# Kernel tuning notes

Hardware: AMD Instinct MI355X
Metric: run time of the kernel (lower is better)

The kernel has to match this reference:

```python
import jax, jax.numpy as jnp
import numpy as np

B, T, N, C, K = 32, 16, 512, 128, 2


def setup_inputs() -> dict:
    key = jax.random.key(0)
    k1, k2, k3 = jax.random.split(key, 3)
    x = jax.random.normal(k1, (B, T, N, C), dtype=jnp.float32)
    adj = jax.random.uniform(k2, (B, N, N), dtype=jnp.float32)
    lambdas = jnp.ones((K,), dtype=jnp.float32)           # raw lambda params (init 1.0)
    thetas = jax.random.uniform(k3, (K, C, C), dtype=jnp.float32)  # torch.rand init
    return {"x": x, "adj": adj, "lambdas": lambdas, "thetas": thetas}


def _akgcn_layer(x, adj, lam_raw, theta):
    # x: [B,T,N,C], adj: [B,N,N]
    lam = 1.0 + jax.nn.relu(lam_raw)  # actual lambda
    h = jnp.einsum('btnc,cd->btnd', x, theta)
    eye = jnp.eye(adj.shape[-1], dtype=adj.dtype)
    v = ((2.0 * lam - 2.0) / lam) * eye + (2.0 / lam) * adj   # [B,N,N]
    v = v / jnp.sum(v, axis=-1, keepdims=True)                 # row-normalize
    out = jnp.einsum('bnm,btmd->btnd', v, h)                   # vectorized over T
    return jax.nn.relu(out)


def reference(x, adj, lambdas, thetas):
    hid = x
    for k in range(K):  # small fixed layer count
        hid = _akgcn_layer(hid, adj, lambdas[k], thetas[k])
    return jax.nn.relu(x) + jax.nn.sigmoid(hid)
```

## Files before the change

### kernel.cpp

```cpp
#include <hip/hip_runtime.h>
#include <hip/hip_bf16.h>

#define BB 32
#define TT 16
#define NNODE 512
#define CC 128

typedef __attribute__((ext_vector_type(8))) short bf16x8;
typedef __attribute__((ext_vector_type(4))) short short4_t;
typedef __attribute__((ext_vector_type(4))) float f32x4;

__device__ __forceinline__ short f2bf(float f) {
    __hip_bfloat16 h = __float2bfloat16(f);
    return *reinterpret_cast<short*>(&h);
}

#define GLD16(g, l)                                                          \
    __builtin_amdgcn_global_load_lds(                                        \
        (const __attribute__((address_space(1))) unsigned int*)(g),          \
        (__attribute__((address_space(3))) unsigned int*)(l), 16, 0, 0)

__global__ void invs_kernel(const float* __restrict__ adj,
                            const float* __restrict__ lambdas, int layer,
                            float* __restrict__ invs) {
    int gid = blockIdx.x * blockDim.x + threadIdx.x;
    int row = gid >> 6;
    int lane = gid & 63;
    const float* r = adj + (long)row * NNODE;
    float s = 0.f;
#pragma unroll
    for (int i = 0; i < NNODE / 64; ++i) s += r[lane + 64 * i];
#pragma unroll
    for (int o = 32; o; o >>= 1) s += __shfl_xor(s, o, 64);
    if (lane == 0) {
        float lamm1 = fmaxf(lambdas[layer], 0.f);
        invs[row] = 1.f / (s + lamm1);
    }
}

__global__ void prep_adj_kernel(const float* __restrict__ adj,
                                const float* __restrict__ invs,
                                const float* __restrict__ lambdas, int layer,
                                short* __restrict__ Abf) {
    long e = ((long)blockIdx.x * 256 + threadIdx.x) * 8;
    int m = (int)(e & (NNODE - 1));
    int n = (int)((e >> 9) & (NNODE - 1));
    int b = (int)(e >> 18);
    float lamm1 = fmaxf(lambdas[layer], 0.f);
    float s = invs[b * NNODE + n];
    float4 f0 = *(const float4*)(adj + e);
    float4 f1 = *(const float4*)(adj + e + 4);
    float vv[8] = {f0.x, f0.y, f0.z, f0.w, f1.x, f1.y, f1.z, f1.w};
#pragma unroll
    for (int j = 0; j < 8; ++j) vv[j] *= s;
    int d = n - m;
    if (d >= 0 && d < 8) vv[d] += lamm1 * s;
    bf16x8 o;
#pragma unroll
    for (int j = 0; j < 8; ++j) o[j] = f2bf(vv[j]);
    *(bf16x8*)(&Abf[e]) = o;
}

__global__ void prep_theta_kernel(const float* __restrict__ theta,
                                  short* __restrict__ thT) {
    int idx = blockIdx.x * 256 + threadIdx.x;
    int i = idx >> 7, k = idx & (CC - 1);
    thT[i * CC + k] = f2bf(theta[k * CC + i]);
}

__global__ __launch_bounds__(256) void gemm_theta_mfma(
    const float* __restrict__ X, const short* __restrict__ thT,
    short* __restrict__ Ht) {
    __shared__ short As[128 * 32];
    __shared__ short Bs[128 * 32];
    const int t = threadIdx.x;
    const long rowBase = (long)blockIdx.x * 128;
    const int w = t >> 6, ln = t & 63;
    const int lm = ln & 15, q = ln >> 4;
    const int wy = w >> 1, wx = w & 1;

    f32x4 acc[4][4] = {};

    const int rr = w * 32 + (ln >> 2);
    const int kc = (ln & 3) * 8;
    short* ldsB = Bs + w * 1024 + ln * 8;

    for (int k0 = 0; k0 < CC; k0 += 32) {
        __syncthreads();
        const short* gb = thT + rr * CC + k0 + kc;
        GLD16(gb, ldsB);
        GLD16(gb + 16 * CC, ldsB + 512);
#pragma unroll
        for (int i = 0; i < 4; ++i) {
            int v = i * 256 + t;
            int r = v >> 3, kq = v & 7;
            float4 f = *(const float4*)(X + (rowBase + r) * CC + k0 + kq * 4);
            short4_t s = {f2bf(f.x), f2bf(f.y), f2bf(f.z), f2bf(f.w)};
            *(short4_t*)(&As[r * 32 + kq * 4]) = s;
        }
        __syncthreads();

        bf16x8 a[4], b[4];
#pragma unroll
        for (int i = 0; i < 4; ++i)
            a[i] = *(const bf16x8*)(&As[(wy * 64 + i * 16 + lm) * 32 + q * 8]);
#pragma unroll
        for (int j = 0; j < 4; ++j)
            b[j] = *(const bf16x8*)(&Bs[(wx * 64 + j * 16 + lm) * 32 + q * 8]);
#pragma unroll
        for (int i = 0; i < 4; ++i)
#pragma unroll
            for (int j = 0; j < 4; ++j)
                acc[i][j] = __builtin_amdgcn_mfma_f32_16x16x32_bf16(
                    a[i], b[j], acc[i][j], 0, 0, 0);
    }

    const long bt = rowBase >> 9;
    const int mBase = (int)(rowBase & (NNODE - 1));
    short* Hb = Ht + bt * (long)(NNODE * CC);
#pragma unroll
    for (int i = 0; i < 4; ++i) {
        int m = mBase + wy * 64 + i * 16 + q * 4;
#pragma unroll
        for (int j = 0; j < 4; ++j) {
            int c = wx * 64 + j * 16 + lm;
            f32x4 v = acc[i][j];
            short4_t s = {f2bf(v[0]), f2bf(v[1]), f2bf(v[2]), f2bf(v[3])};
            *(short4_t*)(&Hb[(long)c * NNODE + m]) = s;
        }
    }
}

template <int FUSE>
__global__ __launch_bounds__(256) void gemm_agg_mfma(
    const short* __restrict__ Abf, const short* __restrict__ Ht,
    const float* __restrict__ x, float* __restrict__ Out) {
    __shared__ short As[128 * 32];
    __shared__ short Bs[128 * 32];
    const int t = threadIdx.x;
    const int bt = blockIdx.y;
    const int n0 = blockIdx.x * 128;
    const short* Ab = Abf + (long)(bt >> 4) * NNODE * NNODE + (long)n0 * NNODE;
    const short* Hb = Ht + (long)bt * NNODE * CC;
    const int w = t >> 6, ln = t & 63;
    const int lm = ln & 15, q = ln >> 4;
    const int wy = w >> 1, wx = w & 1;

    f32x4 acc[4][4] = {};

    const int rr = w * 32 + (ln >> 2);
    const int kc = (ln & 3) * 8;
    short* ldsA = As + w * 1024 + ln * 8;
    short* ldsB = Bs + w * 1024 + ln * 8;

    for (int k0 = 0; k0 < NNODE; k0 += 32) {
        __syncthreads();
        const short* ga = Ab + (long)rr * NNODE + k0 + kc;
        const short* gb = Hb + (long)rr * NNODE + k0 + kc;
        GLD16(ga, ldsA);
        GLD16(ga + 16 * NNODE, ldsA + 512);
        GLD16(gb, ldsB);
        GLD16(gb + 16 * NNODE, ldsB + 512);
        __syncthreads();

        bf16x8 a[4], b[4];
#pragma unroll
        for (int i = 0; i < 4; ++i)
            a[i] = *(const bf16x8*)(&As[(wy * 64 + i * 16 + lm) * 32 + q * 8]);
#pragma unroll
        for (int j = 0; j < 4; ++j)
            b[j] = *(const bf16x8*)(&Bs[(wx * 64 + j * 16 + lm) * 32 + q * 8]);
#pragma unroll
        for (int i = 0; i < 4; ++i)
#pragma unroll
            for (int j = 0; j < 4; ++j)
                acc[i][j] = __builtin_amdgcn_mfma_f32_16x16x32_bf16(
                    a[i], b[j], acc[i][j], 0, 0, 0);
    }

    const long obase = (long)bt * NNODE * CC;
#pragma unroll
    for (int i = 0; i < 4; ++i) {
        int n = n0 + wy * 64 + i * 16 + q * 4;
#pragma unroll
        for (int j = 0; j < 4; ++j) {
            int c = wx * 64 + j * 16 + lm;
#pragma unroll
            for (int r = 0; r < 4; ++r) {
                long idx = obase + (long)(n + r) * CC + c;
                float v = fmaxf(acc[i][j][r], 0.f);
                if (FUSE) {
                    Out[idx] = fmaxf(x[idx], 0.f) + 1.f / (1.f + __expf(-v));
                } else {
                    Out[idx] = v;
                }
            }
        }
    }
}

extern "C" void kernel_launch(void* const* d_in, const int* in_sizes, int n_in,
                              void* d_out, int out_size, void* d_ws,
                              size_t ws_size, hipStream_t stream) {
    const float* x = (const float*)d_in[0];
    const float* adj = (const float*)d_in[1];
    const float* lambdas = (const float*)d_in[2];
    const float* thetas = (const float*)d_in[3];
    float* out = (float*)d_out;

    float* invs = (float*)d_ws;
    short* thT = (short*)(invs + BB * NNODE);
    short* Abf = thT + CC * CC;
    short* Ht = Abf + (long)BB * NNODE * NNODE;

    dim3 blk(256);
    dim3 g_pre(4096);
    dim3 g_theta(2048);
    dim3 g_agg(NNODE / 128, BB * TT);

    invs_kernel<<<g_pre, blk, 0, stream>>>(adj, lambdas, 0, invs);
    prep_adj_kernel<<<g_pre, blk, 0, stream>>>(adj, invs, lambdas, 0, Abf);
    prep_theta_kernel<<<64, blk, 0, stream>>>(thetas, thT);
    gemm_theta_mfma<<<g_theta, blk, 0, stream>>>(x, thT, Ht);
    gemm_agg_mfma<0><<<g_agg, blk, 0, stream>>>(Abf, Ht, out, out);

    invs_kernel<<<g_pre, blk, 0, stream>>>(adj, lambdas, 1, invs);
    prep_adj_kernel<<<g_pre, blk, 0, stream>>>(adj, invs, lambdas, 1, Abf);
    prep_theta_kernel<<<64, blk, 0, stream>>>(thetas + CC * CC, thT);
    gemm_theta_mfma<<<g_theta, blk, 0, stream>>>(out, thT, Ht);
    gemm_agg_mfma<1><<<g_agg, blk, 0, stream>>>(Abf, Ht, x, out);
}
```

Before: 476.6 us.

## Fuse layer-1 aggregation with layer-2 theta GEMM and merge adjacency prep kernels

Merges the row-sum and normalize/convert kernels for the adjacency into one wave-per-row kernel, so adj is read once per layer instead of twice. Fuses the first aggregation GEMM with the second layer's theta GEMM: the ReLU'd tile is staged in LDS as bf16 and multiplied by theta2 in the same block. This removes the fp32 intermediate write and re-read and one full GEMM launch. It uses the output buffer as bf16 scratch for the first H, adds extra LDS (Ts tile), and adds one more rounding to bf16 of the intermediate.

```diff
diff --git a/kernel.cpp b/kernel.cpp
--- a/kernel.cpp
+++ b/kernel.cpp
@@ -20,45 +20,33 @@
         (const __attribute__((address_space(1))) unsigned int*)(g),          \
         (__attribute__((address_space(3))) unsigned int*)(l), 16, 0, 0)
 
-__global__ void invs_kernel(const float* __restrict__ adj,
-                            const float* __restrict__ lambdas, int layer,
-                            float* __restrict__ invs) {
+__global__ void prep_adj2_kernel(const float* __restrict__ adj,
+                                 const float* __restrict__ lambdas, int layer,
+                                 short* __restrict__ Abf) {
     int gid = blockIdx.x * blockDim.x + threadIdx.x;
     int row = gid >> 6;
     int lane = gid & 63;
+    int n = row & (NNODE - 1);
     const float* r = adj + (long)row * NNODE;
-    float s = 0.f;
-#pragma unroll
-    for (int i = 0; i < NNODE / 64; ++i) s += r[lane + 64 * i];
+    float4 f0 = *(const float4*)(r + lane * 4);
+    float4 f1 = *(const float4*)(r + 256 + lane * 4);
+    float s = f0.x + f0.y + f0.z + f0.w + f1.x + f1.y + f1.z + f1.w;
 #pragma unroll
     for (int o = 32; o; o >>= 1) s += __shfl_xor(s, o, 64);
-    if (lane == 0) {
-        float lamm1 = fmaxf(lambdas[layer], 0.f);
-        invs[row] = 1.f / (s + lamm1);
-    }
-}
-
-__global__ void prep_adj_kernel(const float* __restrict__ adj,
-                                const float* __restrict__ invs,
-                                const float* __restrict__ lambdas, int layer,
-                                short* __restrict__ Abf) {
-    long e = ((long)blockIdx.x * 256 + threadIdx.x) * 8;
-    int m = (int)(e & (NNODE - 1));
-    int n = (int)((e >> 9) & (NNODE - 1));
-    int b = (int)(e >> 18);
     float lamm1 = fmaxf(lambdas[layer], 0.f);
-    float s = invs[b * NNODE + n];
-    float4 f0 = *(const float4*)(adj + e);
-    float4 f1 = *(const float4*)(adj + e + 4);
-    float vv[8] = {f0.x, f0.y, f0.z, f0.w, f1.x, f1.y, f1.z, f1.w};
-#pragma unroll
-    for (int j = 0; j < 8; ++j) vv[j] *= s;
-    int d = n - m;
-    if (d >= 0 && d < 8) vv[d] += lamm1 * s;
-    bf16x8 o;
-#pragma unroll
-    for (int j = 0; j < 8; ++j) o[j] = f2bf(vv[j]);
-    *(bf16x8*)(&Abf[e]) = o;
+    float inv = 1.f / (s + lamm1);
+    float v[8] = {f0.x, f0.y, f0.z, f0.w, f1.x, f1.y, f1.z, f1.w};
+#pragma unroll
+    for (int j = 0; j < 8; ++j) v[j] *= inv;
+    int d0 = n - lane * 4;
+    if (d0 >= 0 && d0 < 4) v[d0] += lamm1 * inv;
+    int d1 = n - 256 - lane * 4;
+    if (d1 >= 0 && d1 < 4) v[4 + d1] += lamm1 * inv;
+    short* o = Abf + (long)row * NNODE;
+    short4_t s0 = {f2bf(v[0]), f2bf(v[1]), f2bf(v[2]), f2bf(v[3])};
+    short4_t s1 = {f2bf(v[4]), f2bf(v[5]), f2bf(v[6]), f2bf(v[7])};
+    *(short4_t*)(o + lane * 4) = s0;
+    *(short4_t*)(o + 256 + lane * 4) = s1;
 }
 
 __global__ void prep_theta_kernel(const float* __restrict__ theta,
@@ -127,6 +115,99 @@
             f32x4 v = acc[i][j];
             short4_t s = {f2bf(v[0]), f2bf(v[1]), f2bf(v[2]), f2bf(v[3])};
             *(short4_t*)(&Hb[(long)c * NNODE + m]) = s;
+        }
+    }
+}
+
+__global__ __launch_bounds__(256) void gemm_agg_theta(
+    const short* __restrict__ Abf, const short* __restrict__ Ht1,
+    const short* __restrict__ thT2, short* __restrict__ Ht2) {
+    __shared__ short As[128 * 32];
+    __shared__ short Bs[128 * 32];
+    __shared__ short Ts[128][136];
+    const int t = threadIdx.x;
+    const int bt = blockIdx.y;
+    const int n0 = blockIdx.x * 128;
+    const short* Ab = Abf + (long)(bt >> 4) * NNODE * NNODE + (long)n0 * NNODE;
+    const short* Hb = Ht1 + (long)bt * NNODE * CC;
+    const int w = t >> 6, ln = t & 63;
+    const int lm = ln & 15, q = ln >> 4;
+    const int wy = w >> 1, wx = w & 1;
+
+    f32x4 acc[4][4] = {};
+
+    const int rr = w * 32 + (ln >> 2);
+    const int kc = (ln & 3) * 8;
+    short* ldsA = As + w * 1024 + ln * 8;
+    short* ldsB = Bs + w * 1024 + ln * 8;
+
+    for (int k0 = 0; k0 < NNODE; k0 += 32) {
+        __syncthreads();
+        const short* ga = Ab + (long)rr * NNODE + k0 + kc;
+        const short* gb = Hb + (long)rr * NNODE + k0 + kc;
+        GLD16(ga, ldsA);
+        GLD16(ga + 16 * NNODE, ldsA + 512);
+        GLD16(gb, ldsB);
+        GLD16(gb + 16 * NNODE, ldsB + 512);
+        __syncthreads();
+
+        bf16x8 a[4], b[4];
+#pragma unroll
+        for (int i = 0; i < 4; ++i)
+            a[i] = *(const bf16x8*)(&As[(wy * 64 + i * 16 + lm) * 32 + q * 8]);
+#pragma unroll
+        for (int j = 0; j < 4; ++j)
+            b[j] = *(const bf16x8*)(&Bs[(wx * 64 + j * 16 + lm) * 32 + q * 8]);
+#pragma unroll
+        for (int i = 0; i < 4; ++i)
+#pragma unroll
+            for (int j = 0; j < 4; ++j)
+                acc[i][j] = __builtin_amdgcn_mfma_f32_16x16x32_bf16(
+                    a[i], b[j], acc[i][j], 0, 0, 0);
+    }
+
+#pragma unroll
+    for (int i = 0; i < 4; ++i)
+#pragma unroll
+        for (int j = 0; j < 4; ++j)
+#pragma unroll
+            for (int r = 0; r < 4; ++r)
+                Ts[wy * 64 + i * 16 + q * 4 + r][wx * 64 + j * 16 + lm] =
+                    f2bf(fmaxf(acc[i][j][r], 0.f));
+
+    f32x4 acc2[4][4] = {};
+    for (int c0 = 0; c0 < CC; c0 += 32) {
+        __syncthreads();
+        const short* gb = thT2 + rr * CC + c0 + kc;
+        GLD16(gb, ldsB);
+        GLD16(gb + 16 * CC, ldsB + 512);
+        __syncthreads();
+
+        bf16x8 a[4], b[4];
+#pragma unroll
+        for (int i = 0; i < 4; ++i)
+            a[i] = *(const bf16x8*)(&Ts[wy * 64 + i * 16 + lm][c0 + q * 8]);
+#pragma unroll
+        for (int j = 0; j < 4; ++j)
+            b[j] = *(const bf16x8*)(&Bs[(wx * 64 + j * 16 + lm) * 32 + q * 8]);
+#pragma unroll
+        for (int i = 0; i < 4; ++i)
+#pragma unroll
+            for (int j = 0; j < 4; ++j)
+                acc2[i][j] = __builtin_amdgcn_mfma_f32_16x16x32_bf16(
+                    a[i], b[j], acc2[i][j], 0, 0, 0);
+    }
+
+    short* Hb2 = Ht2 + (long)bt * NNODE * CC;
+#pragma unroll
+    for (int i = 0; i < 4; ++i) {
+        int m = n0 + wy * 64 + i * 16 + q * 4;
+#pragma unroll
+        for (int j = 0; j < 4; ++j) {
+            int c = wx * 64 + j * 16 + lm;
+            f32x4 v = acc2[i][j];
+            short4_t sv = {f2bf(v[0]), f2bf(v[1]), f2bf(v[2]), f2bf(v[3])};
+            *(short4_t*)(&Hb2[(long)c * NNODE + m]) = sv;
         }
     }
 }
@@ -208,25 +289,23 @@
     const float* thetas = (const float*)d_in[3];
     float* out = (float*)d_out;
 
-    float* invs = (float*)d_ws;
-    short* thT = (short*)(invs + BB * NNODE);
-    short* Abf = thT + CC * CC;
-    short* Ht = Abf + (long)BB * NNODE * NNODE;
+    short* Abf = (short*)d_ws;
+    short* Ht2 = Abf + (long)BB * NNODE * NNODE;
+    short* thT0 = Ht2 + (long)BB * TT * NNODE * CC;
+    short* thT1 = thT0 + CC * CC;
+    short* Ht1 = (short*)out;
 
     dim3 blk(256);
-    dim3 g_pre(4096);
-    dim3 g_theta(2048);
     dim3 g_agg(NNODE / 128, BB * TT);
 
-    invs_kernel<<<g_pre, blk, 0, stream>>>(adj, lambdas, 0, invs);
-    prep_adj_kernel<<<g_pre, blk, 0, stream>>>(adj, invs, lambdas, 0, Abf);
-    prep_theta_kernel<<<64, blk, 0, stream>>>(thetas, thT);
-    gemm_theta_mfma<<<g_theta, blk, 0, stream>>>(x, thT, Ht);
-    gemm_agg_mfma<0><<<g_agg, blk, 0, stream>>>(Abf, Ht, out, out);
-
-    invs_kernel<<<g_pre, blk, 0, stream>>>(adj, lambdas, 1, invs);
-    prep_adj_kernel<<<g_pre, blk, 0, stream>>>(adj, invs, lambdas, 1, Abf);
-    prep_theta_kernel<<<64, blk, 0, stream>>>(thetas + CC * CC, thT);
-    gemm_theta_mfma<<<g_theta, blk, 0, stream>>>(out, thT, Ht);
-    gemm_agg_mfma<1><<<g_agg, blk, 0, stream>>>(Abf, Ht, x, out);
-}
+    prep_adj2_kernel<<<4096, blk, 0, stream>>>(adj, lambdas, 0, Abf);
+    prep_theta_kernel<<<64, blk, 0, stream>>>(thetas, thT0);
+    prep_theta_kernel<<<64, blk, 0, stream>>>(thetas + CC * CC, thT1);
+
+    gemm_theta_mfma<<<2048, blk, 0, stream>>>(x, thT0, Ht1);
+
+    gemm_agg_theta<<<g_agg, blk, 0, stream>>>(Abf, Ht1, thT1, Ht2);
+
+    prep_adj2_kernel<<<4096, blk, 0, stream>>>(adj, lambdas, 1, Abf);
+    gemm_agg_mfma<1><<<g_agg, blk, 0, stream>>>(Abf, Ht2, x, out);
+}
```

Measured after the change: 434.1 us. 1.1x faster.
